# Kernel optimization log

Hardware: AMD Instinct MI355X
Metric: run time of the kernel (lower is better)

The kernel has to match this reference:

```python
import jax, jax.numpy as jnp
import numpy as np

C = 64
SIZE = 448
PATCH = 14
P2 = PATCH * PATCH                 # 196, per-chunk token count
SPLIT = (SIZE * SIZE) // P2        # 1024 chunks
TG = PATCH * 4                     # 56, pooled global resolution
POOL = SIZE // TG                  # 8, exact avg-pool factor
EPS = 1e-5


def setup_inputs() -> dict:
    key = jax.random.key(0)
    ks = jax.random.split(key, 10)
    b = 2
    x = jax.random.normal(ks[0], (b, C, SIZE, SIZE), dtype=jnp.float32)
    s = 1.0 / np.sqrt(C)
    return {
        "x": x,
        "gn_w": jnp.ones((C,), jnp.float32),
        "gn_b": jnp.zeros((C,), jnp.float32),
        "q_w": jax.random.normal(ks[1], (C, C), jnp.float32) * s,
        "q_b": jnp.zeros((C,), jnp.float32),
        "k_w": jax.random.normal(ks[2], (C, C), jnp.float32) * s,
        "k_b": jnp.zeros((C,), jnp.float32),
        "v_w": jax.random.normal(ks[3], (C, C), jnp.float32) * s,
        "v_b": jnp.zeros((C,), jnp.float32),
        "proj_w": jax.random.normal(ks[4], (C, C), jnp.float32) * s,
    }


def _conv1x1(t, W, bias=None):
    out = jnp.einsum('oc,bchw->bohw', W, t)
    if bias is not None:
        out = out + bias[None, :, None, None]
    return out


def _group_norm(x, w, b):
    # GroupNorm(num_groups=1): normalize over (C,H,W) per sample
    mean = x.mean(axis=(1, 2, 3), keepdims=True)
    var = x.var(axis=(1, 2, 3), keepdims=True)
    xn = (x - mean) * jax.lax.rsqrt(var + EPS)
    return xn * w[None, :, None, None] + b[None, :, None, None]


def reference(x, gn_w, gn_b, q_w, q_b, k_w, k_b, v_w, v_b, proj_w):
    b, c, h, w = x.shape
    xn = _group_norm(x, gn_w, gn_b)
    q = _conv1x1(xn, q_w, q_b)
    k = _conv1x1(xn, k_w, k_b)
    v = _conv1x1(xn, v_w, v_b)

    # ---- patch-local attention (channels*chunks as feature dim S) ----
    S = c * SPLIT  # 65536
    qf = q.reshape(b, S, P2)
    kf = k.reshape(b, S, P2)
    vf = v.reshape(b, S, P2)
    wm = jnp.einsum('bsp,bsq->bpq', qf, kf) * (S ** -0.5)  # [b,196,196]
    wm = jax.nn.softmax(wm, axis=2)
    # h[b,s,q'] = sum_k v[b,s,k] * wm[b,q',k]
    hp = jnp.einsum('bsk,bqk->bsq', vf, wm).reshape(b, c, h, w)

    # ---- global pooled attention ----
    pool = lambda t: t.reshape(b, c, TG, POOL, TG, POOL).mean(axis=(3, 5))
    qg = pool(q).reshape(b, c, TG * TG)
    kg = pool(k).reshape(b, c, TG * TG)
    vg = pool(v).reshape(b, c, TG * TG)
    wg = jnp.einsum('bcp,bcq->bpq', qg, kg) * (c ** -0.5)  # [b,3136,3136]
    wg = jax.nn.softmax(wg, axis=2)
    hg = jnp.einsum('bck,bqk->bcq', vg, wg).reshape(b, c, TG, TG)
    hg = jnp.repeat(jnp.repeat(hg, POOL, axis=2), POOL, axis=3)

    h_in = 0.75 * hp + 0.25 * hg
    out = _conv1x1(h_in, proj_w)  # proj_out, no bias
    return x + out
```

## Files before the change

### kernel.cpp

```cpp
#include <hip/hip_runtime.h>

#define NB 2
#define NC 64
#define HW 200704
#define CHW 12845056
#define P2 196
#define NCHUNK 1024
#define NCELL 3136
#define WMN 38416

typedef __attribute__((ext_vector_type(8))) short bfrag;
typedef __attribute__((ext_vector_type(4))) float ffrag;
typedef __attribute__((ext_vector_type(4))) short short4v;
typedef __attribute__((ext_vector_type(4))) float float4v;

#define MFMA16(A,B,C) __builtin_amdgcn_mfma_f32_16x16x32_bf16(A,B,C,0,0,0)

__device__ __forceinline__ short f2bf(float f) {
  unsigned u = __builtin_bit_cast(unsigned, f);
  u = u + 0x7FFFu + ((u >> 16) & 1u);
  return (short)(u >> 16);
}

__global__ __launch_bounds__(256) void k0_fold(
    const float* __restrict__ pw, const float* __restrict__ vw,
    const float* __restrict__ vb, float* __restrict__ wtld, float* __restrict__ btld) {
  int t = threadIdx.x;
  if (blockIdx.x == 0) {
    #pragma unroll
    for (int i = 0; i < 16; ++i) {
      int idx = i*256 + t;
      int o = idx >> 6, c = idx & 63;
      float s = 0.f;
      for (int m = 0; m < 64; ++m) s += pw[o*64 + m] * vw[m*64 + c];
      wtld[o*64 + c] = s;
    }
  } else {
    if (t < 64) {
      float s = 0.f;
      for (int m = 0; m < 64; ++m) s += pw[t*64 + m] * vb[m];
      btld[t] = s;
    }
  }
}

__global__ __launch_bounds__(64) void k1_stats_pool(
    const float* __restrict__ x, float* __restrict__ xpool, float* __restrict__ partials) {
  int bx = blockIdx.x;
  int batch = bx / (64*56);
  int c = (bx / 56) % 64;
  int pr = bx % 56;
  int l = threadIdx.x;
  const float* xp = x + (size_t)batch*CHW + (size_t)c*HW + pr*8*448;
  float cell = 0.f, s2 = 0.f;
  if (l < 56) {
    #pragma unroll
    for (int r = 0; r < 8; ++r) {
      float4v a = *(const float4v*)(xp + r*448 + l*8);
      float4v b = *(const float4v*)(xp + r*448 + l*8 + 4);
      #pragma unroll
      for (int j = 0; j < 4; ++j) { cell += a[j] + b[j]; s2 += a[j]*a[j] + b[j]*b[j]; }
    }
    xpool[((size_t)batch*64 + c)*NCELL + pr*56 + l] = cell * (1.f/64.f);
  }
  float s1 = (l < 56) ? cell : 0.f;
  #pragma unroll
  for (int m = 1; m < 64; m <<= 1) { s1 += __shfl_xor(s1, m, 64); s2 += __shfl_xor(s2, m, 64); }
  if (l == 0) { partials[bx*2] = s1; partials[bx*2 + 1] = s2; }
}

__global__ __launch_bounds__(256) void k1b_reduce(
    const float* __restrict__ partials, float* __restrict__ stats) {
  __shared__ float red[2][256];
  int t = threadIdx.x;
  for (int b = 0; b < NB; ++b) {
    float s1 = 0.f, s2 = 0.f;
    for (int i = t; i < 3584; i += 256) {
      s1 += partials[(b*3584 + i)*2];
      s2 += partials[(b*3584 + i)*2 + 1];
    }
    red[0][t] = s1; red[1][t] = s2;
    __syncthreads();
    for (int m = 128; m > 0; m >>= 1) {
      if (t < m) { red[0][t] += red[0][t+m]; red[1][t] += red[1][t+m]; }
      __syncthreads();
    }
    if (t == 0) { stats[b*2] = red[0][0]; stats[b*2+1] = red[1][0]; }
    __syncthreads();
  }
}

__global__ __launch_bounds__(256) void k2_qkv(
    const float* __restrict__ x, const float* __restrict__ gnw, const float* __restrict__ gnb,
    const float* __restrict__ qw, const float* __restrict__ qb,
    const float* __restrict__ kw, const float* __restrict__ kb,
    const float* __restrict__ vw, const float* __restrict__ vb,
    const float* __restrict__ stats,
    short* __restrict__ qx, short* __restrict__ kx, short* __restrict__ vnat) {
  __shared__ __attribute__((aligned(16))) short xnt[256*72];
  int bx = blockIdx.x;
  int batch = bx / 784;
  int px0 = (bx % 784) * 256;
  int t = threadIdx.x;
  float s1 = stats[batch*2], s2 = stats[batch*2+1];
  float mean = s1 * (1.f/CHW);
  float rstd = rsqrtf(s2*(1.f/CHW) - mean*mean + 1e-5f);
  for (int it = 0; it < 64; it += 4) {
    float vv[4];
    #pragma unroll
    for (int r = 0; r < 4; ++r) {
      float v = x[(size_t)batch*CHW + (size_t)(it+r)*HW + px0 + t];
      vv[r] = (v - mean) * rstd * gnw[it+r] + gnb[it+r];
    }
    short4v s;
    #pragma unroll
    for (int r = 0; r < 4; ++r) s[r] = f2bf(vv[r]);
    *(short4v*)(xnt + t*72 + it) = s;
  }
  __syncthreads();
  int l = t & 63, w = t >> 6, li = l & 15, q_ = l >> 4;
  bfrag bfr[4][2];
  #pragma unroll
  for (int nn = 0; nn < 4; ++nn) {
    int row = (w*4 + nn)*16 + li;
    bfr[nn][0] = *(const bfrag*)(xnt + row*72 + q_*8);
    bfr[nn][1] = *(const bfrag*)(xnt + row*72 + 32 + q_*8);
  }
  const float* Ws[3] = {qw, kw, vw};
  const float* Bs[3] = {qb, kb, vb};
  for (int T = 0; T < 3; ++T) {
    ffrag acc[4][4];
    #pragma unroll
    for (int mt = 0; mt < 4; ++mt) {
      bfrag a0, a1;
      const float* wp = Ws[T] + (mt*16 + li)*64;
      #pragma unroll
      for (int j = 0; j < 8; ++j) { a0[j] = f2bf(wp[q_*8 + j]); a1[j] = f2bf(wp[32 + q_*8 + j]); }
      #pragma unroll
      for (int nn = 0; nn < 4; ++nn) {
        ffrag z = {0.f,0.f,0.f,0.f};
        z = MFMA16(a0, bfr[nn][0], z);
        z = MFMA16(a1, bfr[nn][1], z);
        acc[mt][nn] = z;
      }
    }
    if (T < 2) {
      short* dstb = (T == 0 ? qx : kx) + (size_t)batch*HW*64;
      #pragma unroll
      for (int nn = 0; nn < 4; ++nn) {
        int px = px0 + (w*4 + nn)*16 + li;
        #pragma unroll
        for (int mt = 0; mt < 4; ++mt) {
          float4v bias = *(const float4v*)(Bs[T] + mt*16 + q_*4);
          short4v s;
          #pragma unroll
          for (int r = 0; r < 4; ++r) s[r] = f2bf(acc[mt][nn][r] + bias[r]);
          *(short4v*)(dstb + (size_t)px*64 + mt*16 + q_*4) = s;
        }
      }
    } else {
      #pragma unroll
      for (int nn = 0; nn < 4; ++nn) {
        int px = px0 + (w*4 + nn)*16 + li;
        #pragma unroll
        for (int mt = 0; mt < 4; ++mt) {
          float4v bias = *(const float4v*)(Bs[T] + mt*16 + q_*4);
          #pragma unroll
          for (int r = 0; r < 4; ++r) {
            int c = mt*16 + q_*4 + r;
            vnat[((size_t)batch*64 + c)*HW + px] = f2bf(acc[mt][nn][r] + bias[r]);
          }
        }
      }
    }
  }
}

__global__ __launch_bounds__(256) void k2a_pool_qkv(
    const float* __restrict__ xpool, const float* __restrict__ stats,
    const float* __restrict__ gnw, const float* __restrict__ gnb,
    const float* __restrict__ qw, const float* __restrict__ qb,
    const float* __restrict__ kw, const float* __restrict__ kb,
    const float* __restrict__ vw, const float* __restrict__ vb,
    short* __restrict__ qgt, short* __restrict__ kgt, short* __restrict__ vgn) {
  __shared__ float xs[64][64];
  int bx = blockIdx.x;
  int batch = bx / 49;
  int j0 = (bx % 49) * 64;
  int t = threadIdx.x;
  float s1 = stats[batch*2], s2 = stats[batch*2+1];
  float mean = s1 * (1.f/CHW);
  float rstd = rsqrtf(s2*(1.f/CHW) - mean*mean + 1e-5f);
  #pragma unroll
  for (int it = 0; it < 16; ++it) {
    int idx = t + it*256;
    int c = idx >> 6, jl = idx & 63;
    float v = xpool[((size_t)batch*64 + c)*NCELL + j0 + jl];
    xs[c][jl] = (v - mean)*rstd*gnw[c] + gnb[c];
  }
  __syncthreads();
  int jl = t & 63;
  int og = (t >> 6) * 16;
  int j = j0 + jl;
  for (int T = 0; T < 3; ++T) {
    const float* W  = (T==0 ? qw : (T==1 ? kw : vw));
    const float* Bv = (T==0 ? qb : (T==1 ? kb : vb));
    float o16[16];
    #pragma unroll
    for (int oo = 0; oo < 16; ++oo) o16[oo] = Bv[og+oo];
    for (int c = 0; c < 64; ++c) {
      float xv = xs[c][jl];
      #pragma unroll
      for (int oo = 0; oo < 16; ++oo) o16[oo] += W[(og+oo)*64 + c] * xv;
    }
    if (T < 2) {
      short* dst = (T==0 ? qgt : kgt) + ((size_t)batch*NCELL + j)*64 + og;
      #pragma unroll
      for (int oo = 0; oo < 16; oo += 4) {
        short4v s;
        #pragma unroll
        for (int r = 0; r < 4; ++r) s[r] = f2bf(o16[oo+r]);
        *(short4v*)(dst + oo) = s;
      }
    } else {
      #pragma unroll
      for (int oo = 0; oo < 16; ++oo)
        vgn[((size_t)batch*64 + og + oo)*NCELL + j] = f2bf(o16[oo]);
    }
  }
}

__global__ __launch_bounds__(512) void k3_wm(
    const short* __restrict__ qx, const short* __restrict__ kx, float* __restrict__ wmacc) {
  int bx = blockIdx.x;
  int batch = bx >> 7;
  int slab = bx & 127;
  int t = threadIdx.x;
  int l = t & 63, w = t >> 6, li = l & 15, q_ = l >> 4;
  int wm_ = w >> 2, wn = w & 3;
  int m0 = wm_ * 7, mcnt = wm_ ? 6 : 7;
  int nt0 = wn ? 4 + (wn-1)*3 : 0, ncnt = wn ? 3 : 4;
  ffrag acc[7][4];
  #pragma unroll
  for (int i = 0; i < 7; ++i)
    #pragma unroll
    for (int j = 0; j < 4; ++j) acc[i][j] = (ffrag){0.f,0.f,0.f,0.f};
  const short* qbase = qx + (size_t)batch*HW*64;
  const short* kbase = kx + (size_t)batch*HW*64;
  for (int c8 = 0; c8 < 8; ++c8) {
    int chunk = slab*8 + c8;
    const short* qc = qbase + (size_t)chunk*P2*64;
    const short* kc = kbase + (size_t)chunk*P2*64;
    #pragma unroll
    for (int ks = 0; ks < 2; ++ks) {
      int koff = ks*32 + q_*8;
      bfrag af[7], bf[4];
      #pragma unroll
      for (int mi = 0; mi < 7; ++mi) if (mi < mcnt)
        af[mi] = *(const bfrag*)(qc + (size_t)((m0+mi)*16 + li)*64 + koff);
      #pragma unroll
      for (int ni = 0; ni < 4; ++ni) if (ni < ncnt)
        bf[ni] = *(const bfrag*)(kc + (size_t)((nt0+ni)*16 + li)*64 + koff);
      #pragma unroll
      for (int mi = 0; mi < 7; ++mi) if (mi < mcnt)
        #pragma unroll
        for (int ni = 0; ni < 4; ++ni) if (ni < ncnt)
          acc[mi][ni] = MFMA16(af[mi], bf[ni], acc[mi][ni]);
    }
  }
  float* wdst = wmacc + (size_t)batch*WMN;
  #pragma unroll
  for (int mi = 0; mi < 7; ++mi) if (mi < mcnt)
    #pragma unroll
    for (int ni = 0; ni < 4; ++ni) if (ni < ncnt) {
      int qcol = (nt0+ni)*16 + li;
      if (qcol < 196)
        #pragma unroll
        for (int r = 0; r < 4; ++r) {
          int prow = (m0+mi)*16 + q_*4 + r;
          if (prow < 196) atomicAdd(wdst + prow*196 + qcol, acc[mi][ni][r]);
        }
    }
}

__global__ __launch_bounds__(64) void k4_softmax(
    const float* __restrict__ wmacc, short* __restrict__ P) {
  int bx = blockIdx.x;
  int batch = bx / 208;
  int p = bx % 208;
  int l = threadIdx.x;
  short* prow = P + ((size_t)batch*208 + p)*224;
  if (p >= 196) { for (int j = l; j < 224; j += 64) prow[j] = 0; return; }
  const float* src = wmacc + (size_t)batch*WMN + p*196;
  float v[4]; float mx = -1e30f;
  #pragma unroll
  for (int i = 0; i < 4; ++i) {
    int q = l + i*64;
    v[i] = (q < 196) ? src[q]*(1.f/256.f) : -1e30f;
    mx = fmaxf(mx, v[i]);
  }
  #pragma unroll
  for (int m = 1; m < 64; m <<= 1) mx = fmaxf(mx, __shfl_xor(mx, m, 64));
  float s = 0.f;
  #pragma unroll
  for (int i = 0; i < 4; ++i) { v[i] = __expf(v[i] - mx); s += v[i]; }
  #pragma unroll
  for (int m = 1; m < 64; m <<= 1) s += __shfl_xor(s, m, 64);
  float inv = 1.f / s;
  #pragma unroll
  for (int i = 0; i < 4; ++i) {
    int q = l + i*64;
    if (q < 224) prow[q] = (q < 196) ? f2bf(v[i]*inv) : (short)0;
  }
}

__global__ __launch_bounds__(256) void k5_gattn(
    const short* __restrict__ qgt, const short* __restrict__ kgt,
    const short* __restrict__ vgn, float* __restrict__ hgt) {
  __shared__ __attribute__((aligned(16))) short Pl[4][16][72];
  __shared__ __attribute__((aligned(16))) float alph[4][16];
  __shared__ __attribute__((aligned(16))) float Om[4][16][64];
  __shared__ __attribute__((aligned(16))) float ml[4][2][16];
  int bx = blockIdx.x;
  int batch = bx / 196;
  int i0 = (bx % 196) * 16;
  int t = threadIdx.x;
  int w = t >> 6, l = t & 63, li = l & 15, q_ = l >> 4;
  const short* qg = qgt + (size_t)batch*NCELL*64;
  const short* kg = kgt + (size_t)batch*NCELL*64;
  const short* vg = vgn + (size_t)batch*64*NCELL;
  bfrag bq0 = *(const bfrag*)(qg + (size_t)(i0+li)*64 + q_*8);
  bfrag bq1 = *(const bfrag*)(qg + (size_t)(i0+li)*64 + 32 + q_*8);
  float m_run = -1e30f, l_run = 0.f;
  ffrag oa[4];
  #pragma unroll
  for (int i = 0; i < 4; ++i) oa[i] = (ffrag){0.f,0.f,0.f,0.f};
  for (int jt = w; jt < 49; jt += 4) {
    int j0 = jt*64;
    ffrag st[4];
    #pragma unroll
    for (int mt = 0; mt < 4; ++mt) {
      bfrag a0 = *(const bfrag*)(kg + (size_t)(j0 + mt*16 + li)*64 + q_*8);
      bfrag a1 = *(const bfrag*)(kg + (size_t)(j0 + mt*16 + li)*64 + 32 + q_*8);
      ffrag z = {0.f,0.f,0.f,0.f};
      z = MFMA16(a0, bq0, z);
      z = MFMA16(a1, bq1, z);
      st[mt] = z;
    }
    float mx = -1e30f;
    #pragma unroll
    for (int mt = 0; mt < 4; ++mt)
      #pragma unroll
      for (int r = 0; r < 4; ++r) { st[mt][r] *= 0.125f; mx = fmaxf(mx, st[mt][r]); }
    mx = fmaxf(mx, __shfl_xor(mx, 16, 64));
    mx = fmaxf(mx, __shfl_xor(mx, 32, 64));
    float m_new = fmaxf(m_run, mx);
    float alpha = __expf(m_run - m_new);
    float ps = 0.f;
    short4v pk[4];
    #pragma unroll
    for (int mt = 0; mt < 4; ++mt)
      #pragma unroll
      for (int r = 0; r < 4; ++r) { float e = __expf(st[mt][r] - m_new); ps += e; pk[mt][r] = f2bf(e); }
    ps += __shfl_xor(ps, 16, 64);
    ps += __shfl_xor(ps, 32, 64);
    l_run = l_run*alpha + ps;
    m_run = m_new;
    #pragma unroll
    for (int mt = 0; mt < 4; ++mt) *(short4v*)(&Pl[w][li][mt*16 + q_*4]) = pk[mt];
    alph[w][li] = alpha;
    float4v al = *(const float4v*)(&alph[w][q_*4]);
    #pragma unroll
    for (int nt = 0; nt < 4; ++nt)
      #pragma unroll
      for (int r = 0; r < 4; ++r) oa[nt][r] *= al[r];
    #pragma unroll
    for (int ks = 0; ks < 2; ++ks) {
      bfrag a = *(const bfrag*)(&Pl[w][li][ks*32 + q_*8]);
      #pragma unroll
      for (int nt = 0; nt < 4; ++nt) {
        bfrag b = *(const bfrag*)(vg + (size_t)(nt*16 + li)*NCELL + j0 + ks*32 + q_*8);
        oa[nt] = MFMA16(a, b, oa[nt]);
      }
    }
  }
  ml[w][0][li] = m_run;
  ml[w][1][li] = l_run;
  #pragma unroll
  for (int nt = 0; nt < 4; ++nt)
    #pragma unroll
    for (int r = 0; r < 4; ++r)
      Om[w][q_*4 + r][nt*16 + li] = oa[nt][r];
  __syncthreads();
  int qq = t >> 4, c4 = (t & 15) * 4;
  float m0 = ml[0][0][qq], m1 = ml[1][0][qq], m2 = ml[2][0][qq], m3 = ml[3][0][qq];
  float ms = fmaxf(fmaxf(m0, m1), fmaxf(m2, m3));
  float s0 = __expf(m0 - ms), s1 = __expf(m1 - ms);
  float s2 = __expf(m2 - ms), s3 = __expf(m3 - ms);
  float lt = ml[0][1][qq]*s0 + ml[1][1][qq]*s1 + ml[2][1][qq]*s2 + ml[3][1][qq]*s3;
  float inv = 1.f / lt;
  float sw[4] = {s0, s1, s2, s3};
  float4v o = {0.f, 0.f, 0.f, 0.f};
  #pragma unroll
  for (int w2 = 0; w2 < 4; ++w2) {
    float4v ov = *(const float4v*)(&Om[w2][qq][c4]);
    #pragma unroll
    for (int r = 0; r < 4; ++r) o[r] += ov[r] * sw[w2];
  }
  float4v outv;
  #pragma unroll
  for (int r = 0; r < 4; ++r) outv[r] = o[r] * inv;
  *(float4v*)(hgt + (size_t)batch*NCELL*64 + (size_t)(i0 + qq)*64 + c4) = outv;
}

__global__ __launch_bounds__(256) void k6_hp_out(
    const short* __restrict__ vtld, const short* __restrict__ P,
    const float* __restrict__ hgt,
    const float* __restrict__ x, float* __restrict__ out) {
  __shared__ __attribute__((aligned(16))) float fs[16][204];
  int bx = blockIdx.x;
  int batch = bx >> 10;
  int chunk = bx & 1023;
  int t = threadIdx.x;
  int l = t & 63, w = t >> 6, li = l & 15, q_ = l >> 4;
  int nt0 = w ? 4 + (w-1)*3 : 0;
  int ncnt = w ? 3 : 4;
  const short* Pb = P + (size_t)batch*208*224;
  const short* vbase = vtld + (size_t)batch*64*HW + chunk*P2;
  ffrag acc[4][4];
  #pragma unroll
  for (int i = 0; i < 4; ++i)
    #pragma unroll
    for (int j = 0; j < 4; ++j) acc[i][j] = (ffrag){0.f,0.f,0.f,0.f};
  #pragma unroll
  for (int ks = 0; ks < 7; ++ks) {
    int koff = ks*32 + q_*8;
    bfrag av[4];
    #pragma unroll
    for (int mt = 0; mt < 4; ++mt)
      av[mt] = *(const bfrag*)(vbase + (size_t)(mt*16 + li)*HW + koff);
    #pragma unroll
    for (int ni = 0; ni < 4; ++ni) if (ni < ncnt) {
      bfrag bp = *(const bfrag*)(Pb + (size_t)((nt0+ni)*16 + li)*224 + koff);
      #pragma unroll
      for (int mt = 0; mt < 4; ++mt) acc[mt][ni] = MFMA16(av[mt], bp, acc[mt][ni]);
    }
  }
  int pp[4], cell[4];
  #pragma unroll
  for (int ni = 0; ni < 4; ++ni) {
    pp[ni] = (nt0+ni)*16 + li;
    int g = chunk*P2 + pp[ni];
    cell[ni] = ((g / 448) >> 3)*56 + ((g % 448) >> 3);
  }
  const float* hgb = hgt + (size_t)batch*NCELL*64;
  const float* xb = x + (size_t)batch*CHW;
  float* ob = out + (size_t)batch*CHW;
  #pragma unroll
  for (int mt = 0; mt < 4; ++mt) {
    #pragma unroll
    for (int ni = 0; ni < 4; ++ni) if (ni < ncnt) {
      if (pp[ni] < 196) {
        float4v hgv = *(const float4v*)(hgb + (size_t)cell[ni]*64 + mt*16 + q_*4);
        #pragma unroll
        for (int r = 0; r < 4; ++r)
          fs[q_*4 + r][pp[ni]] = 0.75f*acc[mt][ni][r] + 0.25f*hgv[r];
      }
    }
    __syncthreads();
    for (int idx = t; idx < 784; idx += 256) {
      int c16 = idx / 49, po = idx % 49;
      size_t off = (size_t)(mt*16 + c16)*HW + (size_t)chunk*P2 + po*4;
      float4v xv = *(const float4v*)(xb + off);
      float4v fv = *(const float4v*)(&fs[c16][po*4]);
      float4v o;
      #pragma unroll
      for (int r = 0; r < 4; ++r) o[r] = xv[r] + fv[r];
      *(float4v*)(ob + off) = o;
    }
    __syncthreads();
  }
}

extern "C" void kernel_launch(void* const* d_in, const int* in_sizes, int n_in,
                              void* d_out, int out_size, void* d_ws, size_t ws_size,
                              hipStream_t stream) {
  (void)in_sizes; (void)n_in; (void)out_size; (void)ws_size;
  const float* x   = (const float*)d_in[0];
  const float* gnw = (const float*)d_in[1];
  const float* gnb = (const float*)d_in[2];
  const float* qw  = (const float*)d_in[3];
  const float* qb  = (const float*)d_in[4];
  const float* kw  = (const float*)d_in[5];
  const float* kb  = (const float*)d_in[6];
  const float* vw  = (const float*)d_in[7];
  const float* vb  = (const float*)d_in[8];
  const float* pw  = (const float*)d_in[9];
  float* out = (float*)d_out;
  char* ws = (char*)d_ws;

  short* qx    = (short*)(ws + 0);
  short* kx    = (short*)(ws + 51380224);
  short* vnat  = (short*)(ws + 102760448);
  float* xpool = (float*)(ws + 154140672);
  short* qgt   = (short*)(ws + 155746304);
  short* kgt   = (short*)(ws + 156549120);
  short* vgn   = (short*)(ws + 157351936);
  float* hgt   = (float*)(ws + 158154752);
  short* P     = (short*)(ws + 159760384);
  float* wmacc = (float*)(ws + 159946752);
  float* stats = (float*)(ws + 160254080);
  float* partials = (float*)(ws + 159760384);
  float* wtld = (float*)(ws + 158154752);
  float* btld = (float*)(ws + 158154752 + 16384);

  hipMemsetAsync(ws + 159946752, 0, 307328, stream);
  k0_fold      <<<dim3(2),        dim3(256), 0, stream>>>(pw, vw, vb, wtld, btld);
  k1_stats_pool<<<dim3(NB*64*56), dim3(64),  0, stream>>>(x, xpool, partials);
  k1b_reduce   <<<dim3(1),        dim3(256), 0, stream>>>(partials, stats);
  k2_qkv       <<<dim3(NB*784),   dim3(256), 0, stream>>>(x, gnw, gnb, qw, qb, kw, kb, wtld, btld, stats, qx, kx, vnat);
  k2a_pool_qkv <<<dim3(NB*49),    dim3(256), 0, stream>>>(xpool, stats, gnw, gnb, qw, qb, kw, kb, wtld, btld, qgt, kgt, vgn);
  k3_wm        <<<dim3(NB*128),   dim3(512), 0, stream>>>(qx, kx, wmacc);
  k4_softmax   <<<dim3(NB*208),   dim3(64),  0, stream>>>(wmacc, P);
  k5_gattn     <<<dim3(NB*196),   dim3(256), 0, stream>>>(qgt, kgt, vgn, hgt);
  k6_hp_out    <<<dim3(NB*1024),  dim3(256), 0, stream>>>(vnat, P, hgt, x, out);
}
```

Measured before the change: 637.4 us.

## Stage QKV and V stores through LDS, fold 0.75 into softmax, regrid k3

The q/k/v projection kernel now writes its results into shared memory first and then issues wide, coalesced global stores. Before, it wrote short4 per pixel row for q/k and scattered single 2-byte stores for the channel-major V. The output kernel loads the V chunk into LDS once instead of using strided global fragment loads. It also prefetches x and the pooled global result before the barrier and folds the 0.75 local-attention scale into the softmax normalisation. The Gram kernel processes 16 chunks per block on half as many blocks, trading parallelism for fewer atomic accumulations.

New measurement: 664.4 us. 4.2% more time.

```diff
diff --git a/kernel.cpp b/kernel.cpp
--- a/kernel.cpp
+++ b/kernel.cpp
@@ -12,6 +12,7 @@
 typedef __attribute__((ext_vector_type(8))) short bfrag;
 typedef __attribute__((ext_vector_type(4))) float ffrag;
 typedef __attribute__((ext_vector_type(4))) short short4v;
+typedef __attribute__((ext_vector_type(8))) short short8v;
 typedef __attribute__((ext_vector_type(4))) float float4v;
 
 #define MFMA16(A,B,C) __builtin_amdgcn_mfma_f32_16x16x32_bf16(A,B,C,0,0,0)
@@ -144,33 +145,46 @@
         acc[mt][nn] = z;
       }
     }
+    __syncthreads();
     if (T < 2) {
-      short* dstb = (T == 0 ? qx : kx) + (size_t)batch*HW*64;
       #pragma unroll
       for (int nn = 0; nn < 4; ++nn) {
-        int px = px0 + (w*4 + nn)*16 + li;
-        #pragma unroll
-        for (int mt = 0; mt < 4; ++mt) {
-          float4v bias = *(const float4v*)(Bs[T] + mt*16 + q_*4);
-          short4v s;
-          #pragma unroll
-          for (int r = 0; r < 4; ++r) s[r] = f2bf(acc[mt][nn][r] + bias[r]);
-          *(short4v*)(dstb + (size_t)px*64 + mt*16 + q_*4) = s;
-        }
-      }
-    } else {
-      #pragma unroll
-      for (int nn = 0; nn < 4; ++nn) {
-        int px = px0 + (w*4 + nn)*16 + li;
+        int pxl = (w*4 + nn)*16 + li;
         #pragma unroll
         for (int mt = 0; mt < 4; ++mt) {
           float4v bias = *(const float4v*)(Bs[T] + mt*16 + q_*4);
           #pragma unroll
-          for (int r = 0; r < 4; ++r) {
-            int c = mt*16 + q_*4 + r;
-            vnat[((size_t)batch*64 + c)*HW + px] = f2bf(acc[mt][nn][r] + bias[r]);
-          }
+          for (int r = 0; r < 4; ++r)
+            xnt[pxl*72 + mt*16 + q_*4 + r] = f2bf(acc[mt][nn][r] + bias[r]);
         }
+      }
+      __syncthreads();
+      short* dstb = (T == 0 ? qx : kx) + ((size_t)batch*HW + px0)*64;
+      #pragma unroll
+      for (int i = 0; i < 8; ++i) {
+        int idx = t + i*256;
+        int pxl = idx >> 3, sg = idx & 7;
+        *(short8v*)(dstb + (size_t)pxl*64 + sg*8) = *(const short8v*)(xnt + pxl*72 + sg*8);
+      }
+    } else {
+      #pragma unroll
+      for (int nn = 0; nn < 4; ++nn) {
+        int pxl = (w*4 + nn)*16 + li;
+        #pragma unroll
+        for (int mt = 0; mt < 4; ++mt) {
+          float4v bias = *(const float4v*)(Bs[2] + mt*16 + q_*4);
+          #pragma unroll
+          for (int r = 0; r < 4; ++r)
+            xnt[(mt*16 + q_*4 + r)*264 + pxl] = f2bf(acc[mt][nn][r] + bias[r]);
+        }
+      }
+      __syncthreads();
+      short* dstv = vnat + (size_t)batch*64*HW + px0;
+      #pragma unroll
+      for (int i = 0; i < 16; ++i) {
+        int idx = t + i*256;
+        int c = idx >> 6, seg = idx & 63;
+        *(short4v*)(dstv + (size_t)c*HW + seg*4) = *(const short4v*)(xnt + c*264 + seg*4);
       }
     }
   }
@@ -233,8 +247,8 @@
 __global__ __launch_bounds__(512) void k3_wm(
     const short* __restrict__ qx, const short* __restrict__ kx, float* __restrict__ wmacc) {
   int bx = blockIdx.x;
-  int batch = bx >> 7;
-  int slab = bx & 127;
+  int batch = bx >> 6;
+  int slab = bx & 63;
   int t = threadIdx.x;
   int l = t & 63, w = t >> 6, li = l & 15, q_ = l >> 4;
   int wm_ = w >> 2, wn = w & 3;
@@ -247,8 +261,8 @@
     for (int j = 0; j < 4; ++j) acc[i][j] = (ffrag){0.f,0.f,0.f,0.f};
   const short* qbase = qx + (size_t)batch*HW*64;
   const short* kbase = kx + (size_t)batch*HW*64;
-  for (int c8 = 0; c8 < 8; ++c8) {
-    int chunk = slab*8 + c8;
+  for (int c8 = 0; c8 < 16; ++c8) {
+    int chunk = slab*16 + c8;
     const short* qc = qbase + (size_t)chunk*P2*64;
     const short* kc = kbase + (size_t)chunk*P2*64;
     #pragma unroll
@@ -306,7 +320,7 @@
   for (int i = 0; i < 4; ++i) { v[i] = __expf(v[i] - mx); s += v[i]; }
   #pragma unroll
   for (int m = 1; m < 64; m <<= 1) s += __shfl_xor(s, m, 64);
-  float inv = 1.f / s;
+  float inv = 0.75f / s;
   #pragma unroll
   for (int i = 0; i < 4; ++i) {
     int q = l + i*64;
@@ -417,16 +431,27 @@
     const short* __restrict__ vtld, const short* __restrict__ P,
     const float* __restrict__ hgt,
     const float* __restrict__ x, float* __restrict__ out) {
-  __shared__ __attribute__((aligned(16))) float fs[16][204];
+  __shared__ __attribute__((aligned(16))) short smem[64*232];
+  short* vch = smem;
+  float* fs  = (float*)smem;
   int bx = blockIdx.x;
   int batch = bx >> 10;
   int chunk = bx & 1023;
   int t = threadIdx.x;
+  const short* vsrc = vtld + (size_t)batch*64*HW + chunk*P2;
+  for (int idx = t; idx < 3136; idx += 256) {
+    int c = idx / 49, po = idx % 49;
+    *(short4v*)(vch + c*232 + po*4) = *(const short4v*)(vsrc + (size_t)c*HW + po*4);
+  }
+  for (int idx = t; idx < 448; idx += 256) {
+    int c = idx / 7, po = idx % 7;
+    *(short4v*)(vch + c*232 + 196 + po*4) = (short4v){0,0,0,0};
+  }
+  __syncthreads();
   int l = t & 63, w = t >> 6, li = l & 15, q_ = l >> 4;
   int nt0 = w ? 4 + (w-1)*3 : 0;
   int ncnt = w ? 3 : 4;
   const short* Pb = P + (size_t)batch*208*224;
-  const short* vbase = vtld + (size_t)batch*64*HW + chunk*P2;
   ffrag acc[4][4];
   #pragma unroll
   for (int i = 0; i < 4; ++i)
@@ -437,8 +462,7 @@
     int koff = ks*32 + q_*8;
     bfrag av[4];
     #pragma unroll
-    for (int mt = 0; mt < 4; ++mt)
-      av[mt] = *(const bfrag*)(vbase + (size_t)(mt*16 + li)*HW + koff);
+    for (int mt = 0; mt < 4; ++mt) av[mt] = *(const bfrag*)(vch + (mt*16 + li)*232 + koff);
     #pragma unroll
     for (int ni = 0; ni < 4; ++ni) if (ni < ncnt) {
       bfrag bp = *(const bfrag*)(Pb + (size_t)((nt0+ni)*16 + li)*224 + koff);
@@ -446,37 +470,52 @@
       for (int mt = 0; mt < 4; ++mt) acc[mt][ni] = MFMA16(av[mt], bp, acc[mt][ni]);
     }
   }
-  int pp[4], cell[4];
-  #pragma unroll
-  for (int ni = 0; ni < 4; ++ni) {
-    pp[ni] = (nt0+ni)*16 + li;
-    int g = chunk*P2 + pp[ni];
-    cell[ni] = ((g / 448) >> 3)*56 + ((g % 448) >> 3);
-  }
+  int c16[4], pov[4], hadr[4]; size_t offx[4]; bool act[4];
   const float* hgb = hgt + (size_t)batch*NCELL*64;
+  #pragma unroll
+  for (int j = 0; j < 4; ++j) {
+    int idx = t + j*256;
+    act[j] = idx < 784;
+    int cc = act[j] ? (idx / 49) : 0;
+    int po = act[j] ? (idx % 49) : 0;
+    c16[j] = cc; pov[j] = po;
+    int g = chunk*P2 + po*4;
+    int cell = ((g/448) >> 3)*56 + ((g%448) >> 3);
+    hadr[j] = cell*64 + cc;
+    offx[j] = (size_t)cc*HW + (size_t)chunk*P2 + po*4;
+  }
   const float* xb = x + (size_t)batch*CHW;
   float* ob = out + (size_t)batch*CHW;
+  __syncthreads();
   #pragma unroll
   for (int mt = 0; mt < 4; ++mt) {
     #pragma unroll
     for (int ni = 0; ni < 4; ++ni) if (ni < ncnt) {
-      if (pp[ni] < 196) {
-        float4v hgv = *(const float4v*)(hgb + (size_t)cell[ni]*64 + mt*16 + q_*4);
+      int pp = (nt0+ni)*16 + li;
+      if (pp < 196) {
         #pragma unroll
         for (int r = 0; r < 4; ++r)
-          fs[q_*4 + r][pp[ni]] = 0.75f*acc[mt][ni][r] + 0.25f*hgv[r];
+          fs[(q_*4 + r)*204 + pp] = acc[mt][ni][r];
+      }
+    }
+    float4v xr[4]; float hr[4];
+    #pragma unroll
+    for (int j = 0; j < 4; ++j) {
+      if (act[j]) {
+        xr[j] = *(const float4v*)(xb + (size_t)mt*16*HW + offx[j]);
+        hr[j] = hgb[hadr[j] + mt*16];
       }
     }
     __syncthreads();
-    for (int idx = t; idx < 784; idx += 256) {
-      int c16 = idx / 49, po = idx % 49;
-      size_t off = (size_t)(mt*16 + c16)*HW + (size_t)chunk*P2 + po*4;
-      float4v xv = *(const float4v*)(xb + off);
-      float4v fv = *(const float4v*)(&fs[c16][po*4]);
-      float4v o;
-      #pragma unroll
-      for (int r = 0; r < 4; ++r) o[r] = xv[r] + fv[r];
-      *(float4v*)(ob + off) = o;
+    #pragma unroll
+    for (int j = 0; j < 4; ++j) {
+      if (act[j]) {
+        float4v fv = *(const float4v*)(fs + c16[j]*204 + pov[j]*4);
+        float4v o;
+        #pragma unroll
+        for (int r = 0; r < 4; ++r) o[r] = xr[j][r] + fv[r] + 0.25f*hr[j];
+        *(float4v*)(ob + (size_t)mt*16*HW + offx[j]) = o;
+      }
     }
     __syncthreads();
   }
@@ -520,7 +559,7 @@
   k1b_reduce   <<<dim3(1),        dim3(256), 0, stream>>>(partials, stats);
   k2_qkv       <<<dim3(NB*784),   dim3(256), 0, stream>>>(x, gnw, gnb, qw, qb, kw, kb, wtld, btld, stats, qx, kx, vnat);
   k2a_pool_qkv <<<dim3(NB*49),    dim3(256), 0, stream>>>(xpool, stats, gnw, gnb, qw, qb, kw, kb, wtld, btld, qgt, kgt, vgn);
-  k3_wm        <<<dim3(NB*128),   dim3(512), 0, stream>>>(qx, kx, wmacc);
+  k3_wm        <<<dim3(NB*64),    dim3(512), 0, stream>>>(qx, kx, wmacc);
   k4_softmax   <<<dim3(NB*208),   dim3(64),  0, stream>>>(wmacc, P);
   k5_gattn     <<<dim3(NB*196),   dim3(256), 0, stream>>>(qgt, kgt, vgn, hgt);
   k6_hp_out    <<<dim3(NB*1024),  dim3(256), 0, stream>>>(vnat, P, hgt, x, out);
```
